# Kernel optimization log

Hardware: AMD Instinct MI355X
Metric: run time of the kernel (lower is better)

The kernel has to match this reference:

```python
import jax, jax.numpy as jnp
import numpy as np

NEG_SLOPE = 0.01  # torch F.leaky_relu_ default


def setup_inputs() -> dict:
    key = jax.random.key(0)
    k1, k2, k3, k4, k5 = jax.random.split(key, 5)
    N, Fin, Fout = 8192, 256, 128
    X = jax.random.normal(k1, (N, Fin), dtype=jnp.float32)
    adj = jax.random.randint(k2, (N, N), 0, 2, dtype=jnp.int32)
    W = jax.random.normal(k3, (Fout, Fin), dtype=jnp.float32) * 0.05
    b = jax.random.normal(k4, (Fout,), dtype=jnp.float32) * 0.05
    S = jax.random.normal(k5, (2 * Fout,), dtype=jnp.float32)
    return {"X": X, "adj": adj, "W": W, "b": b, "S": S}


def reference(X, adj, W, b, S):
    # X' = W X + b  -> (N, Fout)
    Xp = X @ W.T + b
    N, Fout = Xp.shape
    S_src, S_dst = S[:Fout], S[Fout:]
    # e_ij = leaky_relu(S . [x'_i ; x'_j]) = leaky_relu(S_src.x'_i + S_dst.x'_j)
    e = jax.nn.leaky_relu(
        (Xp @ S_src)[:, None] + (Xp @ S_dst)[None, :], NEG_SLOPE
    )  # (N, N)
    # neighbor set = nonzero entries of adj row plus self-loop
    mask = (adj != 0) | jnp.eye(N, dtype=bool)
    e = jnp.where(mask, e, -jnp.inf)
    attn = jax.nn.softmax(e, axis=1)  # segment softmax over each row's neighbors
    out = jax.nn.sigmoid(attn @ Xp)  # (N, Fout)
    return out
```

## Files before the change

### kernel.cpp

```cpp
#include <hip/hip_runtime.h>

typedef unsigned short u16;
typedef __attribute__((ext_vector_type(8))) u16 u16x8;
typedef __attribute__((ext_vector_type(8))) __bf16 bf16x8;
typedef __attribute__((ext_vector_type(4))) float f32x4;

#define NN 8192
#define FIN 256
#define FOUT 128

__device__ __forceinline__ u16 f2bf(float f) {
  unsigned u = __float_as_uint(f);
  u += 0x7fffu + ((u >> 16) & 1u);
  return (u16)(u >> 16);
}
__device__ __forceinline__ u16 f2bft(float f) {
  return (u16)(__float_as_uint(f) >> 16);
}
__device__ __forceinline__ float bf2f(u16 s) {
  return __uint_as_float(((unsigned)s) << 16);
}

__global__ __launch_bounds__(256) void k_splitw(const float* __restrict__ W,
                                                u16* __restrict__ Whi,
                                                u16* __restrict__ Wlo) {
  int t = blockIdx.x * 256 + threadIdx.x;
  float w = W[t];
  u16 hi = f2bf(w);
  Whi[t] = hi;
  Wlo[t] = f2bf(w - bf2f(hi));
}

__global__ __launch_bounds__(256) void k_xp(const float* __restrict__ X,
    const u16* __restrict__ Whi, const u16* __restrict__ Wlo,
    const float* __restrict__ bias, const float* __restrict__ S,
    const int* __restrict__ adj,
    u16* __restrict__ Bsw, float* __restrict__ cexpA,
    u16* __restrict__ jebA, u16* __restrict__ jeb2A, float* __restrict__ diagW) {
  __shared__ float Xs[16 * 260];
  __shared__ float Xp[16 * 132];
  __shared__ float Ss[256];
  const int tid = threadIdx.x;
  const int i0 = blockIdx.x * 16;
  Ss[tid] = S[tid];
  {
    int r = tid >> 4, c = (tid & 15) * 16;
    const float* src = X + (size_t)(i0 + r) * FIN + c;
    float* dst = Xs + r * 260 + c;
#pragma unroll
    for (int k = 0; k < 16; k += 4) *(float4*)(dst + k) = *(const float4*)(src + k);
  }
  __syncthreads();

  const int w = tid >> 6, l = tid & 63, li = l & 15, quad = l >> 4;
  f32x4 acc[2];
  acc[0] = f32x4{0.f, 0.f, 0.f, 0.f};
  acc[1] = f32x4{0.f, 0.f, 0.f, 0.f};
  for (int k0 = 0; k0 < FIN; k0 += 32) {
    const float* xp = Xs + li * 260 + k0 + quad * 8;
    float4 xa = *(const float4*)xp;
    float4 xb = *(const float4*)(xp + 4);
    float xv[8] = {xa.x, xa.y, xa.z, xa.w, xb.x, xb.y, xb.z, xb.w};
    u16x8 ahiu, alou;
#pragma unroll
    for (int jj = 0; jj < 8; ++jj) {
      u16 h = f2bf(xv[jj]);
      ahiu[jj] = h;
      alou[jj] = f2bf(xv[jj] - bf2f(h));
    }
    bf16x8 ahi = __builtin_bit_cast(bf16x8, ahiu);
    bf16x8 alo = __builtin_bit_cast(bf16x8, alou);
#pragma unroll
    for (int t2 = 0; t2 < 2; ++t2) {
      int f = (w * 2 + t2) * 16 + li;
      size_t wofs = (size_t)f * FIN + k0 + quad * 8;
      bf16x8 bhi = __builtin_bit_cast(bf16x8, *(const u16x8*)(Whi + wofs));
      bf16x8 blo = __builtin_bit_cast(bf16x8, *(const u16x8*)(Wlo + wofs));
      acc[t2] = __builtin_amdgcn_mfma_f32_16x16x32_bf16(ahi, bhi, acc[t2], 0, 0, 0);
      acc[t2] = __builtin_amdgcn_mfma_f32_16x16x32_bf16(alo, bhi, acc[t2], 0, 0, 0);
      acc[t2] = __builtin_amdgcn_mfma_f32_16x16x32_bf16(ahi, blo, acc[t2], 0, 0, 0);
    }
  }
#pragma unroll
  for (int t2 = 0; t2 < 2; ++t2) {
    int f = (w * 2 + t2) * 16 + li;
    float bv = bias[f];
#pragma unroll
    for (int r = 0; r < 4; ++r)
      Xp[(quad * 4 + r) * 132 + f] = acc[t2][r] + bv;
  }
  __syncthreads();

  {
    int li2 = tid & 15, q2sub = (tid >> 4) & 1, nt = tid >> 5;
    int f = nt * 16 + li2;
    int rb = q2sub * 8;
    int q2 = ((i0 & 16) >> 3) + q2sub;
    u16x8 ou;
#pragma unroll
    for (int jj = 0; jj < 8; ++jj) ou[jj] = f2bf(Xp[(rb + jj) * 132 + f]);
    *(u16x8*)(Bsw + ((size_t)(i0 >> 5) * 8 + nt) * 512 + (size_t)(q2 * 16 + li2) * 8) = ou;
  }

  {
    int r = tid >> 4, sub = tid & 15;
    float pa = 0.f, pb = 0.f;
#pragma unroll
    for (int m = 0; m < 8; ++m) {
      float x = Xp[r * 132 + sub + m * 16];
      pa += x * Ss[sub + m * 16];
      pb += x * Ss[128 + sub + m * 16];
    }
    pa += __shfl_xor(pa, 1); pa += __shfl_xor(pa, 2);
    pa += __shfl_xor(pa, 4); pa += __shfl_xor(pa, 8);
    pb += __shfl_xor(pb, 1); pb += __shfl_xor(pb, 2);
    pb += __shfl_xor(pb, 4); pb += __shfl_xor(pb, 8);
    if (sub == 0) {
      int i = i0 + r;
      float cc = expf(-0.99f * pa);
      u16 ebq = f2bf(expf(pb));
      u16 e2q = f2bf(expf(0.01f * pb));
      cexpA[i] = cc;
      jebA[i] = ebq;
      jeb2A[i] = e2q;
      float wii = fmaxf(bf2f(ebq), cc * bf2f(e2q));
      float wq = bf2f(f2bft(wii));
      int ad = adj[(size_t)i * NN + i];
      diagW[i] = (ad != 0) ? 0.f : wq;
    }
  }
}

__global__ __launch_bounds__(512, 4) void k_gat(const int* __restrict__ adj,
    const u16* __restrict__ Bsw, const float* __restrict__ cexpA,
    const u16* __restrict__ jebA, const u16* __restrict__ jeb2A,
    const float* __restrict__ diagW, float* __restrict__ out) {
  __shared__ float sacc[16 * 132];
  __shared__ float sden[16];
  const int tid = threadIdx.x;
  const int i0 = blockIdx.x * 16;

  {
    int r = tid >> 5, f = (tid & 31) * 4;
    int i = i0 + r;
    float dw = diagW[i];
    size_t slotbase = (size_t)(i0 >> 5) * 8;
    int laneq = ((i & 31) >> 3) * 16;
    int elem = i & 7;
    float4 v;
    float* vp = &v.x;
#pragma unroll
    for (int k = 0; k < 4; ++k) {
      int ff = f + k;
      u16 xb = Bsw[(slotbase + (ff >> 4)) * 512 + (size_t)(laneq + (ff & 15)) * 8 + elem];
      vp[k] = dw * bf2f(xb);
    }
    *(float4*)&sacc[r * 132 + f] = v;
    if (tid < 16) sden[tid] = diagW[i0 + tid];
  }
  __syncthreads();

  const int w = tid >> 6, l = tid & 63, li = l & 15, quad = l >> 4;
  const int im = i0 + li;
  const float c = cexpA[im];
  const int* ar = adj + (size_t)im * NN;

  f32x4 acc[8];
#pragma unroll
  for (int nt = 0; nt < 8; ++nt) acc[nt] = f32x4{0.f, 0.f, 0.f, 0.f};
  f32x4 accD = f32x4{0.f, 0.f, 0.f, 0.f};

  u16x8 onesu;
#pragma unroll
  for (int jj = 0; jj < 8; ++jj) onesu[jj] = 0x3F80;
  const bf16x8 ONES = __builtin_bit_cast(bf16x8, onesu);

  const int jbeg = w * 1024, jend = jbeg + 1024;
  const int qofs = quad * 8;

  int4 ca0, ca1;
  u16x8 ceb, ce2;
  {
    const int jq = jbeg + qofs;
    ca0 = *(const int4*)(ar + jq);
    ca1 = *(const int4*)(ar + jq + 4);
    ceb = *(const u16x8*)(jebA + jq);
    ce2 = *(const u16x8*)(jeb2A + jq);
  }
  for (int j0 = jbeg; j0 < jend; j0 += 32) {
    const int jn = (j0 + 32 < jend) ? (j0 + 32) : jbeg;
    const int jq = jn + qofs;
    int4 na0 = *(const int4*)(ar + jq);
    int4 na1 = *(const int4*)(ar + jq + 4);
    u16x8 neb = *(const u16x8*)(jebA + jq);
    u16x8 ne2 = *(const u16x8*)(jeb2A + jq);

    int av[8] = {ca0.x, ca0.y, ca0.z, ca0.w, ca1.x, ca1.y, ca1.z, ca1.w};
    float wv[8];
#pragma unroll
    for (int jj = 0; jj < 8; ++jj) {
      float ww = fmaxf(bf2f(ceb[jj]), c * bf2f(ce2[jj]));
      wv[jj] = (av[jj] != 0) ? ww : 0.f;
    }
    unsigned pk[4];
#pragma unroll
    for (int p = 0; p < 4; ++p)
      pk[p] = __builtin_amdgcn_perm(__float_as_uint(wv[2 * p + 1]),
                                    __float_as_uint(wv[2 * p]), 0x07060302u);
    bf16x8 A = __builtin_bit_cast(bf16x8, *(u16x8*)pk);

    const u16* bb = Bsw + (size_t)(j0 >> 5) * 4096 + (size_t)l * 8;
#pragma unroll
    for (int nt = 0; nt < 8; ++nt) {
      bf16x8 B = __builtin_bit_cast(bf16x8, *(const u16x8*)(bb + nt * 512));
      acc[nt] = __builtin_amdgcn_mfma_f32_16x16x32_bf16(A, B, acc[nt], 0, 0, 0);
    }
    accD = __builtin_amdgcn_mfma_f32_16x16x32_bf16(A, ONES, accD, 0, 0, 0);

    ca0 = na0; ca1 = na1; ceb = neb; ce2 = ne2;
  }

  if (li == 0) {
#pragma unroll
    for (int r = 0; r < 4; ++r) atomicAdd(&sden[quad * 4 + r], accD[r]);
  }
#pragma unroll
  for (int nt = 0; nt < 8; ++nt) {
#pragma unroll
    for (int r = 0; r < 4; ++r)
      atomicAdd(&sacc[(quad * 4 + r) * 132 + nt * 16 + li], acc[nt][r]);
  }
  __syncthreads();

  {
    int r = tid >> 5, c4 = (tid & 31) * 4;
    float4 v = *(const float4*)&sacc[r * 132 + c4];
    float rd = 1.f / sden[r];
    float o[4] = {v.x, v.y, v.z, v.w};
#pragma unroll
    for (int k = 0; k < 4; ++k) {
      float t = o[k] * rd;
      o[k] = 1.f / (1.f + __expf(-t));
    }
    *(float4*)(out + (size_t)(i0 + r) * FOUT + c4) = make_float4(o[0], o[1], o[2], o[3]);
  }
}

extern "C" void kernel_launch(void* const* d_in, const int* in_sizes, int n_in,
                              void* d_out, int out_size, void* d_ws, size_t ws_size,
                              hipStream_t stream) {
  const float* X = (const float*)d_in[0];
  const int* adj = (const int*)d_in[1];
  const float* W = (const float*)d_in[2];
  const float* bias = (const float*)d_in[3];
  const float* S = (const float*)d_in[4];
  float* out = (float*)d_out;

  char* ws = (char*)d_ws;
  u16* Bsw      = (u16*)(ws);
  u16* Whi      = (u16*)(ws + 2097152);
  u16* Wlo      = (u16*)(ws + 2162688);
  float* cexpA  = (float*)(ws + 2228224);
  u16* jebA     = (u16*)(ws + 2260992);
  u16* jeb2A    = (u16*)(ws + 2277376);
  float* diagW  = (float*)(ws + 2293760);

  hipLaunchKernelGGL(k_splitw, dim3(128), dim3(256), 0, stream, W, Whi, Wlo);
  hipLaunchKernelGGL(k_xp, dim3(512), dim3(256), 0, stream, X, Whi, Wlo, bias, S, adj,
                     Bsw, cexpA, jebA, jeb2A, diagW);
  hipLaunchKernelGGL(k_gat, dim3(512), dim3(512), 0, stream, adj, Bsw, cexpA,
                     jebA, jeb2A, diagW, out);
}
```

Before: 476.8 us.

## Stage adjacency weights through double-buffered LDS with coalesced row loads

```diff
diff --git a/kernel.cpp b/kernel.cpp
--- a/kernel.cpp
+++ b/kernel.cpp
@@ -8,6 +8,9 @@
 #define NN 8192
 #define FIN 256
 #define FOUT 128
+#define PW 512
+#define NP (NN / PW)
+#define WSTRIDE 520
 
 __device__ __forceinline__ u16 f2bf(float f) {
   unsigned u = __float_as_uint(f);
@@ -135,10 +138,12 @@
     const u16* __restrict__ Bsw, const float* __restrict__ cexpA,
     const u16* __restrict__ jebA, const u16* __restrict__ jeb2A,
     const float* __restrict__ diagW, float* __restrict__ out) {
+  __shared__ u16 wb[2][16 * WSTRIDE];
   __shared__ float sacc[16 * 132];
   __shared__ float sden[16];
   const int tid = threadIdx.x;
   const int i0 = blockIdx.x * 16;
+  const int w = tid >> 6, l = tid & 63, li = l & 15, quad = l >> 4;
 
   {
     int r = tid >> 5, f = (tid & 31) * 4;
@@ -158,66 +163,84 @@
     *(float4*)&sacc[r * 132 + f] = v;
     if (tid < 16) sden[tid] = diagW[i0 + tid];
   }
-  __syncthreads();
-
-  const int w = tid >> 6, l = tid & 63, li = l & 15, quad = l >> 4;
-  const int im = i0 + li;
-  const float c = cexpA[im];
-  const int* ar = adj + (size_t)im * NN;
+
+  const int r0 = 2 * w;
+  const float c0 = cexpA[i0 + r0];
+  const float c1 = cexpA[i0 + r0 + 1];
+  const int* arow0 = adj + (size_t)(i0 + r0) * NN;
+  const int* arow1 = arow0 + NN;
+
+  int4 pa[4];
+  ushort4 teb[2], te2[2];
+
+  auto stage_load = [&](int p) {
+    int base = p * PW + l * 4;
+#pragma unroll
+    for (int k = 0; k < 2; ++k) {
+      pa[k * 2]     = *(const int4*)(arow0 + base + k * 256);
+      pa[k * 2 + 1] = *(const int4*)(arow1 + base + k * 256);
+      teb[k] = *(const ushort4*)(jebA + base + k * 256);
+      te2[k] = *(const ushort4*)(jeb2A + base + k * 256);
+    }
+  };
+
+  auto stage_store = [&](int buf) {
+#pragma unroll
+    for (int r2 = 0; r2 < 2; ++r2) {
+      float cr = r2 ? c1 : c0;
+#pragma unroll
+      for (int k = 0; k < 2; ++k) {
+        const int* av = (const int*)&pa[k * 2 + r2];
+        const u16* ebp = (const u16*)&teb[k];
+        const u16* e2p = (const u16*)&te2[k];
+        float wv[4];
+#pragma unroll
+        for (int e = 0; e < 4; ++e) {
+          float ww = fmaxf(bf2f(ebp[e]), cr * bf2f(e2p[e]));
+          wv[e] = (av[e] != 0) ? ww : 0.f;
+        }
+        unsigned p0 = __builtin_amdgcn_perm(__float_as_uint(wv[1]),
+                                            __float_as_uint(wv[0]), 0x07060302u);
+        unsigned p1 = __builtin_amdgcn_perm(__float_as_uint(wv[3]),
+                                            __float_as_uint(wv[2]), 0x07060302u);
+        *(uint2*)&wb[buf][(r0 + r2) * WSTRIDE + k * 256 + l * 4] = make_uint2(p0, p1);
+      }
+    }
+  };
 
   f32x4 acc[8];
 #pragma unroll
   for (int nt = 0; nt < 8; ++nt) acc[nt] = f32x4{0.f, 0.f, 0.f, 0.f};
   f32x4 accD = f32x4{0.f, 0.f, 0.f, 0.f};
-
   u16x8 onesu;
 #pragma unroll
   for (int jj = 0; jj < 8; ++jj) onesu[jj] = 0x3F80;
   const bf16x8 ONES = __builtin_bit_cast(bf16x8, onesu);
 
-  const int jbeg = w * 1024, jend = jbeg + 1024;
-  const int qofs = quad * 8;
-
-  int4 ca0, ca1;
-  u16x8 ceb, ce2;
-  {
-    const int jq = jbeg + qofs;
-    ca0 = *(const int4*)(ar + jq);
-    ca1 = *(const int4*)(ar + jq + 4);
-    ceb = *(const u16x8*)(jebA + jq);
-    ce2 = *(const u16x8*)(jeb2A + jq);
-  }
-  for (int j0 = jbeg; j0 < jend; j0 += 32) {
-    const int jn = (j0 + 32 < jend) ? (j0 + 32) : jbeg;
-    const int jq = jn + qofs;
-    int4 na0 = *(const int4*)(ar + jq);
-    int4 na1 = *(const int4*)(ar + jq + 4);
-    u16x8 neb = *(const u16x8*)(jebA + jq);
-    u16x8 ne2 = *(const u16x8*)(jeb2A + jq);
-
-    int av[8] = {ca0.x, ca0.y, ca0.z, ca0.w, ca1.x, ca1.y, ca1.z, ca1.w};
-    float wv[8];
-#pragma unroll
-    for (int jj = 0; jj < 8; ++jj) {
-      float ww = fmaxf(bf2f(ceb[jj]), c * bf2f(ce2[jj]));
-      wv[jj] = (av[jj] != 0) ? ww : 0.f;
-    }
-    unsigned pk[4];
-#pragma unroll
-    for (int p = 0; p < 4; ++p)
-      pk[p] = __builtin_amdgcn_perm(__float_as_uint(wv[2 * p + 1]),
-                                    __float_as_uint(wv[2 * p]), 0x07060302u);
-    bf16x8 A = __builtin_bit_cast(bf16x8, *(u16x8*)pk);
-
-    const u16* bb = Bsw + (size_t)(j0 >> 5) * 4096 + (size_t)l * 8;
-#pragma unroll
-    for (int nt = 0; nt < 8; ++nt) {
-      bf16x8 B = __builtin_bit_cast(bf16x8, *(const u16x8*)(bb + nt * 512));
-      acc[nt] = __builtin_amdgcn_mfma_f32_16x16x32_bf16(A, B, acc[nt], 0, 0, 0);
-    }
-    accD = __builtin_amdgcn_mfma_f32_16x16x32_bf16(A, ONES, accD, 0, 0, 0);
-
-    ca0 = na0; ca1 = na1; ceb = neb; ce2 = ne2;
+  auto compute = [&](int p, int buf) {
+#pragma unroll
+    for (int t = 0; t < 2; ++t) {
+      int s = w * 2 + t;
+      u16x8 au = *(const u16x8*)&wb[buf][li * WSTRIDE + s * 32 + quad * 8];
+      bf16x8 A = __builtin_bit_cast(bf16x8, au);
+      const u16* bb = Bsw + (size_t)(p * 16 + s) * 4096 + (size_t)l * 8;
+#pragma unroll
+      for (int nt = 0; nt < 8; ++nt) {
+        bf16x8 B = __builtin_bit_cast(bf16x8, *(const u16x8*)(bb + nt * 512));
+        acc[nt] = __builtin_amdgcn_mfma_f32_16x16x32_bf16(A, B, acc[nt], 0, 0, 0);
+      }
+      accD = __builtin_amdgcn_mfma_f32_16x16x32_bf16(A, ONES, accD, 0, 0, 0);
+    }
+  };
+
+  stage_load(0);
+  stage_store(0);
+  __syncthreads();
+  for (int p = 0; p < NP; ++p) {
+    if (p + 1 < NP) stage_load(p + 1);
+    compute(p, p & 1);
+    if (p + 1 < NP) stage_store((p + 1) & 1);
+    __syncthreads();
   }
 
   if (li == 0) {
```

Result: faster. 442.7 us (-7.1%).

## Precompute bitmask from adjacency and process 32 rows per attention block

Applied to the files above, without the earlier changes.

```diff
diff --git a/kernel.cpp b/kernel.cpp
--- a/kernel.cpp
+++ b/kernel.cpp
@@ -1,6 +1,7 @@
 #include <hip/hip_runtime.h>
 
 typedef unsigned short u16;
+typedef unsigned char u8;
 typedef __attribute__((ext_vector_type(8))) u16 u16x8;
 typedef __attribute__((ext_vector_type(8))) __bf16 bf16x8;
 typedef __attribute__((ext_vector_type(4))) float f32x4;
@@ -29,6 +30,30 @@
   u16 hi = f2bf(w);
   Whi[t] = hi;
   Wlo[t] = f2bf(w - bf2f(hi));
+}
+
+__global__ __launch_bounds__(256) void k_mask(const int* __restrict__ adj,
+                                              u8* __restrict__ mask) {
+  const int wave_id = blockIdx.x * 4 + (threadIdx.x >> 6);
+  const int l = threadIdx.x & 63;
+#pragma unroll 1
+  for (int it = 0; it < 32; ++it) {
+    int g = wave_id + it * 4096;
+    int row = g >> 4, cir = g & 15;
+    const int* p = adj + (size_t)row * NN + cir * 512 + l * 8;
+    int4 a = *(const int4*)p;
+    int4 b = *(const int4*)(p + 4);
+    unsigned m = 0;
+    m |= min((unsigned)a.x, 1u);
+    m |= min((unsigned)a.y, 1u) << 1;
+    m |= min((unsigned)a.z, 1u) << 2;
+    m |= min((unsigned)a.w, 1u) << 3;
+    m |= min((unsigned)b.x, 1u) << 4;
+    m |= min((unsigned)b.y, 1u) << 5;
+    m |= min((unsigned)b.z, 1u) << 6;
+    m |= min((unsigned)b.w, 1u) << 7;
+    mask[(size_t)row * 1024 + cir * 64 + l] = (u8)m;
+  }
 }
 
 __global__ __launch_bounds__(256) void k_xp(const float* __restrict__ X,
@@ -131,118 +156,121 @@
   }
 }
 
-__global__ __launch_bounds__(512, 4) void k_gat(const int* __restrict__ adj,
+__global__ __launch_bounds__(512, 3) void k_gat(const u8* __restrict__ mask,
     const u16* __restrict__ Bsw, const float* __restrict__ cexpA,
     const u16* __restrict__ jebA, const u16* __restrict__ jeb2A,
     const float* __restrict__ diagW, float* __restrict__ out) {
-  __shared__ float sacc[16 * 132];
-  __shared__ float sden[16];
+  __shared__ float sacc[32 * 132];
+  __shared__ float sden[32];
   const int tid = threadIdx.x;
-  const int i0 = blockIdx.x * 16;
-
-  {
-    int r = tid >> 5, f = (tid & 31) * 4;
+  const int i0 = blockIdx.x * 32;
+
+  {
+    int r = tid >> 4, f8 = (tid & 15) * 8;
     int i = i0 + r;
     float dw = diagW[i];
-    size_t slotbase = (size_t)(i0 >> 5) * 8;
-    int laneq = ((i & 31) >> 3) * 16;
-    int elem = i & 7;
-    float4 v;
-    float* vp = &v.x;
-#pragma unroll
-    for (int k = 0; k < 4; ++k) {
-      int ff = f + k;
-      u16 xb = Bsw[(slotbase + (ff >> 4)) * 512 + (size_t)(laneq + (ff & 15)) * 8 + elem];
-      vp[k] = dw * bf2f(xb);
-    }
-    *(float4*)&sacc[r * 132 + f] = v;
-    if (tid < 16) sden[tid] = diagW[i0 + tid];
+    int jblk = i >> 5, q2 = (i & 31) >> 3, jj = i & 7;
+#pragma unroll
+    for (int k = 0; k < 8; ++k) {
+      int ff = f8 + k;
+      u16 xb = Bsw[((size_t)jblk * 8 + (ff >> 4)) * 512 +
+                   (size_t)(q2 * 16 + (ff & 15)) * 8 + jj];
+      sacc[r * 132 + ff] = dw * bf2f(xb);
+    }
+    if (tid < 32) sden[tid] = diagW[i0 + tid];
   }
   __syncthreads();
 
   const int w = tid >> 6, l = tid & 63, li = l & 15, quad = l >> 4;
-  const int im = i0 + li;
-  const float c = cexpA[im];
-  const int* ar = adj + (size_t)im * NN;
-
-  f32x4 acc[8];
-#pragma unroll
-  for (int nt = 0; nt < 8; ++nt) acc[nt] = f32x4{0.f, 0.f, 0.f, 0.f};
-  f32x4 accD = f32x4{0.f, 0.f, 0.f, 0.f};
-
+  const float c0 = cexpA[i0 + li];
+  const float c1 = cexpA[i0 + 16 + li];
+  const u8* mp0 = mask + (size_t)(i0 + li) * 1024;
+  const u8* mp1 = mp0 + 16 * 1024;
+
+  f32x4 acc0[8], acc1[8];
+#pragma unroll
+  for (int nt = 0; nt < 8; ++nt) {
+    acc0[nt] = f32x4{0.f, 0.f, 0.f, 0.f};
+    acc1[nt] = f32x4{0.f, 0.f, 0.f, 0.f};
+  }
+  f32x4 accD0 = f32x4{0.f, 0.f, 0.f, 0.f};
+  f32x4 accD1 = f32x4{0.f, 0.f, 0.f, 0.f};
   u16x8 onesu;
 #pragma unroll
   for (int jj = 0; jj < 8; ++jj) onesu[jj] = 0x3F80;
   const bf16x8 ONES = __builtin_bit_cast(bf16x8, onesu);
 
-  const int jbeg = w * 1024, jend = jbeg + 1024;
-  const int qofs = quad * 8;
-
-  int4 ca0, ca1;
-  u16x8 ceb, ce2;
-  {
-    const int jq = jbeg + qofs;
-    ca0 = *(const int4*)(ar + jq);
-    ca1 = *(const int4*)(ar + jq + 4);
-    ceb = *(const u16x8*)(jebA + jq);
-    ce2 = *(const u16x8*)(jeb2A + jq);
-  }
-  for (int j0 = jbeg; j0 < jend; j0 += 32) {
-    const int jn = (j0 + 32 < jend) ? (j0 + 32) : jbeg;
-    const int jq = jn + qofs;
-    int4 na0 = *(const int4*)(ar + jq);
-    int4 na1 = *(const int4*)(ar + jq + 4);
-    u16x8 neb = *(const u16x8*)(jebA + jq);
-    u16x8 ne2 = *(const u16x8*)(jeb2A + jq);
-
-    int av[8] = {ca0.x, ca0.y, ca0.z, ca0.w, ca1.x, ca1.y, ca1.z, ca1.w};
-    float wv[8];
-#pragma unroll
-    for (int jj = 0; jj < 8; ++jj) {
-      float ww = fmaxf(bf2f(ceb[jj]), c * bf2f(ce2[jj]));
-      wv[jj] = (av[jj] != 0) ? ww : 0.f;
-    }
-    unsigned pk[4];
-#pragma unroll
-    for (int p = 0; p < 4; ++p)
-      pk[p] = __builtin_amdgcn_perm(__float_as_uint(wv[2 * p + 1]),
-                                    __float_as_uint(wv[2 * p]), 0x07060302u);
-    bf16x8 A = __builtin_bit_cast(bf16x8, *(u16x8*)pk);
-
-    const u16* bb = Bsw + (size_t)(j0 >> 5) * 4096 + (size_t)l * 8;
+  const int ks0 = w * 32;
+  for (int s = 0; s < 32; ++s) {
+    const int ks = ks0 + s;
+    const int jq = ks * 32 + quad * 8;
+    int mb0 = mp0[ks * 4 + quad];
+    int mb1 = mp1[ks * 4 + quad];
+    u16x8 ceb = *(const u16x8*)(jebA + jq);
+    u16x8 ce2 = *(const u16x8*)(jeb2A + jq);
+    float w0[8], w1[8];
+#pragma unroll
+    for (int e = 0; e < 8; ++e) {
+      float eb = bf2f(ceb[e]);
+      float e2 = bf2f(ce2[e]);
+      float a0 = fmaxf(eb, c0 * e2);
+      float a1 = fmaxf(eb, c1 * e2);
+      w0[e] = ((mb0 >> e) & 1) ? a0 : 0.f;
+      w1[e] = ((mb1 >> e) & 1) ? a1 : 0.f;
+    }
+    unsigned p0[4], p1[4];
+#pragma unroll
+    for (int p = 0; p < 4; ++p) {
+      p0[p] = __builtin_amdgcn_perm(__float_as_uint(w0[2 * p + 1]),
+                                    __float_as_uint(w0[2 * p]), 0x07060302u);
+      p1[p] = __builtin_amdgcn_perm(__float_as_uint(w1[2 * p + 1]),
+                                    __float_as_uint(w1[2 * p]), 0x07060302u);
+    }
+    bf16x8 A0 = __builtin_bit_cast(bf16x8, *(u16x8*)p0);
+    bf16x8 A1 = __builtin_bit_cast(bf16x8, *(u16x8*)p1);
+
+    const u16* bb = Bsw + (size_t)ks * 4096 + (size_t)l * 8;
 #pragma unroll
     for (int nt = 0; nt < 8; ++nt) {
       bf16x8 B = __builtin_bit_cast(bf16x8, *(const u16x8*)(bb + nt * 512));
-      acc[nt] = __builtin_amdgcn_mfma_f32_16x16x32_bf16(A, B, acc[nt], 0, 0, 0);
-    }
-    accD = __builtin_amdgcn_mfma_f32_16x16x32_bf16(A, ONES, accD, 0, 0, 0);
-
-    ca0 = na0; ca1 = na1; ceb = neb; ce2 = ne2;
+      acc0[nt] = __builtin_amdgcn_mfma_f32_16x16x32_bf16(A0, B, acc0[nt], 0, 0, 0);
+      acc1[nt] = __builtin_amdgcn_mfma_f32_16x16x32_bf16(A1, B, acc1[nt], 0, 0, 0);
+    }
+    accD0 = __builtin_amdgcn_mfma_f32_16x16x32_bf16(A0, ONES, accD0, 0, 0, 0);
+    accD1 = __builtin_amdgcn_mfma_f32_16x16x32_bf16(A1, ONES, accD1, 0, 0, 0);
   }
 
   if (li == 0) {
 #pragma unroll
-    for (int r = 0; r < 4; ++r) atomicAdd(&sden[quad * 4 + r], accD[r]);
+    for (int r = 0; r < 4; ++r) {
+      atomicAdd(&sden[quad * 4 + r], accD0[r]);
+      atomicAdd(&sden[16 + quad * 4 + r], accD1[r]);
+    }
   }
 #pragma unroll
   for (int nt = 0; nt < 8; ++nt) {
 #pragma unroll
-    for (int r = 0; r < 4; ++r)
-      atomicAdd(&sacc[(quad * 4 + r) * 132 + nt * 16 + li], acc[nt][r]);
+    for (int r = 0; r < 4; ++r) {
+      atomicAdd(&sacc[(quad * 4 + r) * 132 + nt * 16 + li], acc0[nt][r]);
+      atomicAdd(&sacc[(16 + quad * 4 + r) * 132 + nt * 16 + li], acc1[nt][r]);
+    }
   }
   __syncthreads();
 
   {
-    int r = tid >> 5, c4 = (tid & 31) * 4;
-    float4 v = *(const float4*)&sacc[r * 132 + c4];
+    int r = tid >> 4, f8 = (tid & 15) * 8;
     float rd = 1.f / sden[r];
-    float o[4] = {v.x, v.y, v.z, v.w};
-#pragma unroll
-    for (int k = 0; k < 4; ++k) {
+    float4 v0 = *(const float4*)&sacc[r * 132 + f8];
+    float4 v1 = *(const float4*)&sacc[r * 132 + f8 + 4];
+    float o[8] = {v0.x, v0.y, v0.z, v0.w, v1.x, v1.y, v1.z, v1.w};
+#pragma unroll
+    for (int k = 0; k < 8; ++k) {
       float t = o[k] * rd;
       o[k] = 1.f / (1.f + __expf(-t));
     }
-    *(float4*)(out + (size_t)(i0 + r) * FOUT + c4) = make_float4(o[0], o[1], o[2], o[3]);
+    float* op = out + (size_t)(i0 + r) * FOUT + f8;
+    *(float4*)op = make_float4(o[0], o[1], o[2], o[3]);
+    *(float4*)(op + 4) = make_float4(o[4], o[5], o[6], o[7]);
   }
 }
 
@@ -264,10 +292,12 @@
   u16* jebA     = (u16*)(ws + 2260992);
   u16* jeb2A    = (u16*)(ws + 2277376);
   float* diagW  = (float*)(ws + 2293760);
-
+  u8* mask      = (u8*)(ws + 2326528);
+
+  hipLaunchKernelGGL(k_mask, dim3(1024), dim3(256), 0, stream, adj, mask);
   hipLaunchKernelGGL(k_splitw, dim3(128), dim3(256), 0, stream, W, Whi, Wlo);
   hipLaunchKernelGGL(k_xp, dim3(512), dim3(256), 0, stream, X, Whi, Wlo, bias, S, adj,
                      Bsw, cexpA, jebA, jeb2A, diagW);
-  hipLaunchKernelGGL(k_gat, dim3(512), dim3(512), 0, stream, adj, Bsw, cexpA,
+  hipLaunchKernelGGL(k_gat, dim3(256), dim3(512), 0, stream, mask, Bsw, cexpA,
                      jebA, jeb2A, diagW, out);
 }
```

Result: slower. 503.7 us (+5.6%).
